# Kernel optimization log

Hardware: AMD Instinct MI355X
Metric: run time of the kernel (lower is better)

Reference implementation:

```python
import jax, jax.numpy as jnp
import numpy as np

N_SAMPLES = 10
DROPOUT_P = 0.1
EPS = 1e-12
B, F, C = 32768, 512, 1000


def setup_inputs() -> dict:
    key = jax.random.key(0)
    k1, k2, k3, k4 = jax.random.split(key, 4)
    return {
        "features": jax.random.normal(k1, (B, F), dtype=jnp.float32),
        "logits": jax.random.normal(k2, (B, C), dtype=jnp.float32),
        "W": jax.random.normal(k3, (F, C), dtype=jnp.float32) * 0.05,
        "b": jax.random.normal(k4, (C,), dtype=jnp.float32) * 0.05,
    }


def reference(features, logits, W, b):
    # `logits` is part of the provider interface but unused by this provider.
    del logits
    keep_p = 1.0 - DROPOUT_P
    mask_key = jax.random.key(42)
    # (n_samples, batch, feat) Bernoulli keep masks; inverted-dropout scaling.
    masks = jax.random.bernoulli(mask_key, keep_p, (N_SAMPLES,) + features.shape)
    dropped = jnp.where(masks, features[None] / keep_p, 0.0)  # (S, B, F)
    lgts = jnp.einsum("sbf,fc->sbc", dropped, W) + b          # (S, B, C)
    probs = jax.nn.softmax(lgts, axis=-1)                      # (S, B, C)
    mean = jnp.mean(probs, axis=0)                             # (B, C)
    # torch .var(dim=0) uses unbiased (n-1) normalization.
    var = jnp.sum((probs - mean[None]) ** 2, axis=0) / (N_SAMPLES - 1)
    total_var = jnp.sum(var, axis=-1, keepdims=True)           # (B, 1)
    # Scaler not fitted -> _normalize is identity.
    return jnp.log(total_var + EPS)
```

## Files before the change

kernel.cpp:

```cpp
#include <hip/hip_runtime.h>
#include <hip/hip_bf16.h>
#include <stdint.h>
#include <math.h>

typedef __attribute__((ext_vector_type(8))) short short8;
typedef __attribute__((ext_vector_type(4))) float f32x4;

namespace {
constexpr int kB = 32768;
constexpr int kF = 512;
constexpr int kC = 1000;
constexpr int kCpad = 1024;
constexpr int kS = 10;
constexpr int G = 8;
constexpr int M = G * kS;
constexpr int MT = M / 16;
constexpr int NTW = 8;
constexpr int WAVES = 8;
constexpr int SK = 64;
constexpr int SLICES = kF / SK;
constexpr uint32_t SLICE_BYTES = M * SK * 2;
constexpr uint32_t kKeepThr = 3865470464u;
}

__device__ __forceinline__ uint32_t rotl32(uint32_t x, uint32_t r) {
#if __has_builtin(__builtin_rotateleft32)
  return __builtin_rotateleft32(x, r);
#else
  return (x << r) | (x >> (32u - r));
#endif
}

__device__ __forceinline__ uint32_t threefry2x32_xor(uint32_t c0, uint32_t c1) {
  const uint32_t ks0 = 0u;
  const uint32_t ks1 = 42u;
  const uint32_t ks2 = 0x1BD11BDAu ^ ks0 ^ ks1;
  uint32_t x0 = c0 + ks0;
  uint32_t x1 = c1 + ks1;
#define TF_ROUND(r) { x0 += x1; x1 = rotl32(x1, r); x1 ^= x0; }
  TF_ROUND(13u) TF_ROUND(15u) TF_ROUND(26u) TF_ROUND(6u)
  x0 += ks1; x1 += ks2 + 1u;
  TF_ROUND(17u) TF_ROUND(29u) TF_ROUND(16u) TF_ROUND(24u)
  x0 += ks2; x1 += ks0 + 2u;
  TF_ROUND(13u) TF_ROUND(15u) TF_ROUND(26u) TF_ROUND(6u)
  x0 += ks0; x1 += ks1 + 3u;
  TF_ROUND(17u) TF_ROUND(29u) TF_ROUND(16u) TF_ROUND(24u)
  x0 += ks1; x1 += ks2 + 4u;
  TF_ROUND(13u) TF_ROUND(15u) TF_ROUND(26u) TF_ROUND(6u)
  x0 += ks2; x1 += ks0 + 5u;
#undef TF_ROUND
  return x0 ^ x1;
}

__device__ __forceinline__ uint32_t f2bf(float x) {
  uint32_t u = __float_as_uint(x);
  return (u + 0x7fffu + ((u >> 16) & 1u)) >> 16;
}

__device__ __forceinline__ uint32_t pack_bf16x2(float lo, float hi) {
  uint32_t r;
  asm("v_cvt_pk_bf16_f32 %0, %1, %2" : "=v"(r) : "v"(lo), "v"(hi));
  return r;
}


__global__ __launch_bounds__(256) void prep_wt(const float* __restrict__ W,
                                               ushort* __restrict__ Wt) {
  __shared__ float tile[64][65];
  const int kt = blockIdx.x * 64;
  const int ct = blockIdx.y * 64;
  const int tid = threadIdx.x;
#pragma unroll
  for (int i = 0; i < 16; ++i) {
    const int lin = i * 256 + tid;
    const int rk = lin >> 6, cc = lin & 63;
    const int gc = ct + cc;
    tile[rk][cc] = (gc < kC) ? W[(size_t)(kt + rk) * kC + gc] : 0.0f;
  }
  __syncthreads();
#pragma unroll
  for (int i = 0; i < 8; ++i) {
    const int lin = i * 256 + tid;
    const int cc = lin >> 5, kp = lin & 31;
    const int gc = ct + cc;
    const uint32_t lo = f2bf(tile[kp * 2][cc]);
    const uint32_t hi = f2bf(tile[kp * 2 + 1][cc]);
    ((uint32_t*)Wt)[(size_t)gc * (kF / 2) + (kt >> 1) + kp] = lo | (hi << 16);
  }
}

__global__ __launch_bounds__(256) void prep_bias(const float* __restrict__ b,
                                                 float* __restrict__ biasp) {
  const int i = blockIdx.x * 256 + threadIdx.x;
  if (i < kCpad) biasp[i] = (i < kC) ? b[i] : -INFINITY;
}


__global__ __launch_bounds__(512, 2) void mc_mfma_kernel(
    const float* __restrict__ features, const ushort* __restrict__ Wt,
    const float* __restrict__ biasp, float* __restrict__ out) {
  __shared__ __align__(16) ushort Abuf[2][M * SK];
  __shared__ float wred[M][9];
  __shared__ float rowinv[M];
  __shared__ float part[G][9];

  const int tid = threadIdx.x;
  const int b0 = blockIdx.x * G;
  const int wv = tid >> 6;
  const int lane = tid & 63;
  const int cp = lane & 15;
  const int gr = lane >> 4;
  const int cbase = wv * 128;

  const int fp = tid & 31;
  const int mbase = tid >> 5;
  const int gg = mbase & 7;
  const int s0 = mbase >> 3;
  char* const Ab0 = (char*)&Abuf[0][0];

  const uint32_t idx_row =
      (uint32_t)s0 * (uint32_t)(kB * kF) + (uint32_t)(b0 + gg) * kF +
      (uint32_t)(fp * 2);
  const uint32_t swz_off =
      ((uint32_t)(mbase * 128 + fp * 4)) ^ ((uint32_t)gg << 4);
  const float2* const fbase =
      (const float2*)features + ((uint32_t)(b0 + gg) * (kF / 2) + fp);

  auto gen_dword = [&](uint32_t idxb, uint32_t byteb, int i, float f0,
                       float f1) {
    const uint32_t c1 = idxb + ((uint32_t)i << 25);
    const uint32_t bits0 = threefry2x32_xor(0u, c1);
    const uint32_t bits1 = threefry2x32_xor(0u, c1 + 1u);
    const float a0 = (bits0 < kKeepThr) ? f0 : 0.0f;
    const float a1 = (bits1 < kKeepThr) ? f1 : 0.0f;
    *(uint32_t*)(Ab0 + byteb + (uint32_t)(i * 2048)) = pack_bf16x2(a0, a1);
  };

  f32x4 acc[MT][NTW];
#pragma unroll
  for (int mt = 0; mt < MT; ++mt)
#pragma unroll
    for (int nt = 0; nt < NTW; ++nt)
#pragma unroll
      for (int r = 0; r < 4; ++r) acc[mt][nt][r] = 0.0f;

  const uint32_t wbase = (uint32_t)(cbase + cp) * kF + (uint32_t)(gr * 8);
  const uint32_t aswz = (uint32_t)((cp & 7) << 4);
  const uint32_t arow = (uint32_t)(cp * 128);

  {
    const float2 fv = fbase[0];
    const float f0 = fv.x * (1.0f / 0.9f);
    const float f1 = fv.y * (1.0f / 0.9f);
#pragma unroll
    for (int i = 0; i < 5; ++i) gen_dword(idx_row, swz_off, i, f0, f1);
  }
  __syncthreads();

#pragma unroll 1
  for (int sl = 0; sl < SLICES; ++sl) {
    const uint32_t cur = (uint32_t)(sl & 1) * SLICE_BYTES;
    const uint32_t nxt = cur ^ SLICE_BYTES;
    const uint32_t wsl = wbase + (uint32_t)(sl * SK);
    const char* Ar = (const char*)Ab0 + cur;
    const bool has_next = (sl + 1 < SLICES);

    const float2 fv = fbase[((sl + 1) & 7) * 32];
    const float f0 = fv.x * (1.0f / 0.9f);
    const float f1 = fv.y * (1.0f / 0.9f);
    const uint32_t idxb = idx_row + (uint32_t)((sl + 1) * SK);
    const uint32_t byteb = nxt + swz_off;

    short8 bfA[4], bfB[4];

#pragma unroll
    for (int nt = 0; nt < 4; ++nt)
      bfA[nt] = *(const short8*)(Wt + wsl + (uint32_t)nt * 8192u);

    if (has_next) {
#pragma unroll
      for (int i = 0; i < 3; ++i) gen_dword(idxb, byteb, i, f0, f1);
    }
    __builtin_amdgcn_sched_barrier(0);

#pragma unroll
    for (int nt = 0; nt < 4; ++nt)
      bfB[nt] = *(const short8*)(Wt + wsl + (uint32_t)(nt + 4) * 8192u);

    short8 a[MT];
#pragma unroll
    for (int mt = 0; mt < MT; ++mt)
      a[mt] = *(const short8*)(Ar + (uint32_t)(mt * 2048) + arow +
                               (((uint32_t)(gr * 16)) ^ aswz));
    __builtin_amdgcn_s_setprio(1);
#pragma unroll
    for (int nt = 0; nt < 4; ++nt)
#pragma unroll
      for (int mt = 0; mt < MT; ++mt)
        acc[mt][nt] = __builtin_amdgcn_mfma_f32_16x16x32_bf16(
            a[mt], bfA[nt], acc[mt][nt], 0, 0, 0);
#pragma unroll
    for (int nt = 4; nt < 8; ++nt)
#pragma unroll
      for (int mt = 0; mt < MT; ++mt)
        acc[mt][nt] = __builtin_amdgcn_mfma_f32_16x16x32_bf16(
            a[mt], bfB[nt - 4], acc[mt][nt], 0, 0, 0);
    __builtin_amdgcn_s_setprio(0);
    __builtin_amdgcn_sched_barrier(0);

#pragma unroll
    for (int nt = 0; nt < 4; ++nt)
      bfA[nt] = *(const short8*)(Wt + wsl + 32u + (uint32_t)nt * 8192u);

    if (has_next) {
#pragma unroll
      for (int i = 3; i < 5; ++i) gen_dword(idxb, byteb, i, f0, f1);
    }
    __builtin_amdgcn_sched_barrier(0);

#pragma unroll
    for (int nt = 0; nt < 4; ++nt)
      bfB[nt] = *(const short8*)(Wt + wsl + 32u + (uint32_t)(nt + 4) * 8192u);

#pragma unroll
    for (int mt = 0; mt < MT; ++mt)
      a[mt] = *(const short8*)(Ar + (uint32_t)(mt * 2048) + arow +
                               (((uint32_t)(64 + gr * 16)) ^ aswz));
    __builtin_amdgcn_s_setprio(1);
#pragma unroll
    for (int nt = 0; nt < 4; ++nt)
#pragma unroll
      for (int mt = 0; mt < MT; ++mt)
        acc[mt][nt] = __builtin_amdgcn_mfma_f32_16x16x32_bf16(
            a[mt], bfA[nt], acc[mt][nt], 0, 0, 0);
#pragma unroll
    for (int nt = 4; nt < 8; ++nt)
#pragma unroll
      for (int mt = 0; mt < MT; ++mt)
        acc[mt][nt] = __builtin_amdgcn_mfma_f32_16x16x32_bf16(
            a[mt], bfB[nt - 4], acc[mt][nt], 0, 0, 0);
    __builtin_amdgcn_s_setprio(0);

    __syncthreads();
  }

  const float* bp = biasp + cbase + cp;
  float bias_lane[NTW];
#pragma unroll
  for (int nt = 0; nt < NTW; ++nt) bias_lane[nt] = bp[nt * 16];

  float red[MT][4];
#pragma unroll
  for (int mt = 0; mt < MT; ++mt)
#pragma unroll
    for (int r = 0; r < 4; ++r) {
      float z = 0.0f;
#pragma unroll
      for (int nt = 0; nt < NTW; ++nt) {
        const float e = __expf(acc[mt][nt][r] + bias_lane[nt]);
        acc[mt][nt][r] = e;
        z += e;
      }
      red[mt][r] = z;
    }
#pragma unroll
  for (int off = 1; off <= 8; off <<= 1)
#pragma unroll
    for (int mt = 0; mt < MT; ++mt)
#pragma unroll
      for (int r = 0; r < 4; ++r) red[mt][r] += __shfl_xor(red[mt][r], off);
  if (cp == 0) {
#pragma unroll
    for (int mt = 0; mt < MT; ++mt)
#pragma unroll
      for (int r = 0; r < 4; ++r) wred[mt * 16 + gr * 4 + r][wv] = red[mt][r];
  }
  __syncthreads();
  if (tid < M) {
    float z = 0.0f;
#pragma unroll
    for (int w = 0; w < WAVES; ++w) z += wred[tid][w];
    rowinv[tid] = 1.0f / z;
  }
  __syncthreads();

#pragma unroll
  for (int mt = 0; mt < MT; ++mt)
#pragma unroll
    for (int r = 0; r < 4; ++r) red[mt][r] = rowinv[mt * 16 + gr * 4 + r];

  float vp[4] = {0.0f, 0.0f, 0.0f, 0.0f};
#pragma unroll
  for (int nt = 0; nt < NTW; ++nt)
#pragma unroll
    for (int r = 0; r < 4; ++r) {
      float sp = 0.0f, sp2 = 0.0f;
#pragma unroll
      for (int mt = 0; mt < MT; ++mt) {
        const float p = acc[mt][nt][r] * red[mt][r];
        sp += p;
        sp2 += p * p;
      }
      sp += __shfl_xor(sp, 32);
      sp2 += __shfl_xor(sp2, 32);
      vp[r] += sp2 - sp * sp * 0.1f;
    }
#pragma unroll
  for (int off = 1; off <= 8; off <<= 1)
#pragma unroll
    for (int r = 0; r < 4; ++r) vp[r] += __shfl_xor(vp[r], off);
  if (cp == 0 && gr < 2) {
#pragma unroll
    for (int r = 0; r < 4; ++r) part[gr * 4 + r][wv] = vp[r];
  }
  __syncthreads();
  if (tid < G) {
    float t = 0.0f;
#pragma unroll
    for (int w = 0; w < WAVES; ++w) t += part[tid][w];
    t = fmaxf(t, 0.0f);
    out[b0 + tid] = logf(t * (1.0f / 9.0f) + 1e-12f);
  }
}


template <bool IS_MAX>
__device__ __forceinline__ float block_reduce(float v, float* red) {
#pragma unroll
  for (int off = 32; off >= 1; off >>= 1) {
    const float o = __shfl_xor(v, off);
    v = IS_MAX ? fmaxf(v, o) : (v + o);
  }
  const int wid = threadIdx.x >> 6;
  if ((threadIdx.x & 63) == 0) red[wid] = v;
  __syncthreads();
  float r = red[0];
#pragma unroll
  for (int w = 1; w < 4; ++w) r = IS_MAX ? fmaxf(r, red[w]) : (r + red[w]);
  __syncthreads();
  return r;
}

__global__ __launch_bounds__(256) void mc_dropout_var_kernel(
    const float* __restrict__ features, const float* __restrict__ W,
    const float* __restrict__ bias, float* __restrict__ out) {
  const int b = blockIdx.x;
  const int tid = threadIdx.x;
  __shared__ float mf[kS][kF];
  __shared__ float red[4];
  const uint32_t row_base = (uint32_t)b * (uint32_t)kF;
  for (int k = 0; k < (kS * kF) / 256; ++k) {
    const int lin = k * 256 + tid;
    const int s = lin >> 9;
    const int f = lin & (kF - 1);
    const uint32_t idx =
        (uint32_t)s * (uint32_t)(kB * kF) + row_base + (uint32_t)f;
    const uint32_t bits = threefry2x32_xor(0u, idx);
    const float u = __uint_as_float((bits >> 9) | 0x3f800000u) - 1.0f;
    const float fv = features[row_base + f];
    mf[s][f] = (u < 0.9f) ? (fv / 0.9f) : 0.0f;
  }
  __syncthreads();
  const bool active = (tid < kC / 4);
  const int c0 = tid * 4;
  float acc[kS][4];
#pragma unroll
  for (int s = 0; s < kS; ++s)
#pragma unroll
    for (int j = 0; j < 4; ++j) acc[s][j] = 0.0f;
  if (active) {
    const float* wp = W + c0;
    for (int f = 0; f < kF; f += 4) {
      float wv[4][4];
      *reinterpret_cast<float4*>(wv[0]) =
          *reinterpret_cast<const float4*>(wp + (size_t)(f + 0) * kC);
      *reinterpret_cast<float4*>(wv[1]) =
          *reinterpret_cast<const float4*>(wp + (size_t)(f + 1) * kC);
      *reinterpret_cast<float4*>(wv[2]) =
          *reinterpret_cast<const float4*>(wp + (size_t)(f + 2) * kC);
      *reinterpret_cast<float4*>(wv[3]) =
          *reinterpret_cast<const float4*>(wp + (size_t)(f + 3) * kC);
#pragma unroll
      for (int s = 0; s < kS; ++s) {
        float mm[4];
        *reinterpret_cast<float4*>(mm) =
            *reinterpret_cast<const float4*>(&mf[s][f]);
#pragma unroll
        for (int j = 0; j < 4; ++j) {
#pragma unroll
          for (int q = 0; q < 4; ++q)
            acc[s][j] = fmaf(mm[q], wv[q][j], acc[s][j]);
        }
      }
    }
  }
  float bias_r[4] = {0.f, 0.f, 0.f, 0.f};
  if (active) {
    const float4 bb = *reinterpret_cast<const float4*>(bias + c0);
    bias_r[0] = bb.x; bias_r[1] = bb.y; bias_r[2] = bb.z; bias_r[3] = bb.w;
  }
  float sum_p[4] = {0.f, 0.f, 0.f, 0.f};
  float sum_p2[4] = {0.f, 0.f, 0.f, 0.f};
#pragma unroll 1
  for (int s = 0; s < kS; ++s) {
    float l[4] = {0.f, 0.f, 0.f, 0.f};
    float lmax = -INFINITY;
    if (active) {
#pragma unroll
      for (int j = 0; j < 4; ++j) {
        l[j] = acc[s][j] + bias_r[j];
        lmax = fmaxf(lmax, l[j]);
      }
    }
    const float bmax = block_reduce<true>(lmax, red);
    float psum = 0.f;
    float p[4] = {0.f, 0.f, 0.f, 0.f};
    if (active) {
#pragma unroll
      for (int j = 0; j < 4; ++j) {
        p[j] = expf(l[j] - bmax);
        psum += p[j];
      }
    }
    const float bsum = block_reduce<false>(psum, red);
    const float inv = 1.0f / bsum;
    if (active) {
#pragma unroll
      for (int j = 0; j < 4; ++j) {
        const float pr = p[j] * inv;
        sum_p[j] += pr;
        sum_p2[j] += pr * pr;
      }
    }
  }
  float partv = 0.f;
  if (active) {
#pragma unroll
    for (int j = 0; j < 4; ++j)
      partv += (sum_p2[j] - sum_p[j] * sum_p[j] * 0.1f) * (1.0f / 9.0f);
  }
  const float total = block_reduce<false>(partv, red);
  if (tid == 0) out[b] = logf(total + 1e-12f);
}


extern "C" void kernel_launch(void* const* d_in, const int* in_sizes, int n_in,
                              void* d_out, int out_size, void* d_ws, size_t ws_size,
                              hipStream_t stream) {
  const float* features = (const float*)d_in[0];
  const float* W = (const float*)d_in[2];
  const float* bias = (const float*)d_in[3];
  float* out = (float*)d_out;

  const size_t wt_bytes = (size_t)kCpad * kF * sizeof(ushort);
  const size_t need = wt_bytes + (size_t)kCpad * sizeof(float);

  if (ws_size >= need) {
    ushort* Wt = (ushort*)d_ws;
    float* biasp = (float*)((char*)d_ws + wt_bytes);
    hipLaunchKernelGGL(prep_wt, dim3(kF / 64, kCpad / 64), dim3(256), 0, stream,
                       W, Wt);
    hipLaunchKernelGGL(prep_bias, dim3((kCpad + 255) / 256), dim3(256), 0,
                       stream, bias, biasp);
    hipLaunchKernelGGL(mc_mfma_kernel, dim3(kB / G), dim3(512), 0, stream,
                       features, Wt, biasp, out);
  } else {
    hipLaunchKernelGGL(mc_dropout_var_kernel, dim3(kB), dim3(256), 0, stream,
                       features, W, bias, out);
  }
}
```

Baseline: 672.7 us.

## Split dropout mask generation into a separate bit-packed PRNG kernel

Adds a standalone kernel that runs Threefry once per mask bit and packs the keep decisions into 32-bit words in workspace (about 21 MB). A new GEMM kernel loads each block's mask words into LDS and expands features with bit tests instead of hashing inline, and it uses larger 128-wide K slices. The aim is to take the integer-heavy PRNG work out of the MFMA main loop so it no longer competes with matrix issue. The cost is an extra launch plus a write and read of the mask buffer through global memory, and the new path only runs when the workspace is large enough.

Result: slower. 1.154 ms (+71.6%).

```diff
diff --git a/kernel.cpp b/kernel.cpp
--- a/kernel.cpp
+++ b/kernel.cpp
@@ -20,6 +20,10 @@
 constexpr int SK = 64;
 constexpr int SLICES = kF / SK;
 constexpr uint32_t SLICE_BYTES = M * SK * 2;
+constexpr int SK2 = 128;
+constexpr int SLICES2 = kF / SK2;
+constexpr uint32_t SLICE_B2 = M * SK2 * 2;
+constexpr uint32_t kMaskWords = (uint32_t)kS * kB * (kF / 32);
 constexpr uint32_t kKeepThr = 3865470464u;
 }
 
@@ -96,6 +100,220 @@
 }
 
 
+__global__ __launch_bounds__(256) void prng_masks(uint32_t* __restrict__ mw) {
+  const uint32_t t = blockIdx.x * 256u + threadIdx.x;
+#pragma unroll 1
+  for (int k = 0; k < 10; ++k) {
+    const uint32_t w = (uint32_t)k * 524288u + t;
+    const uint32_t base = w << 5;
+    uint32_t word = 0u;
+#pragma unroll
+    for (int j = 0; j < 32; ++j)
+      word |= (threefry2x32_xor(0u, base + (uint32_t)j) < kKeepThr)
+                  ? (1u << j)
+                  : 0u;
+    mw[w] = word;
+  }
+}
+
+
+__global__ __launch_bounds__(512, 2) void mc_gemm_kernel(
+    const float* __restrict__ features, const ushort* __restrict__ Wt,
+    const float* __restrict__ biasp, const uint32_t* __restrict__ maskw,
+    float* __restrict__ out) {
+  __shared__ __align__(16) ushort Abuf[2][M * SK2];
+  __shared__ uint32_t mlds[M][16];
+  __shared__ float wred[M][9];
+  __shared__ float rowinv[M];
+  __shared__ float part[G][9];
+
+  const int tid = threadIdx.x;
+  const int b0 = blockIdx.x * G;
+  const int wv = tid >> 6;
+  const int lane = tid & 63;
+  const int cp = lane & 15;
+  const int gr = lane >> 4;
+  const int cbase = wv * 128;
+  char* const Ab0 = (char*)&Abuf[0][0];
+
+  for (int w = tid; w < M * 16; w += 512) {
+    const int m = w >> 4, ww = w & 15;
+    mlds[m][ww] = maskw[((uint32_t)(m >> 3) << 19) +
+                        (uint32_t)(b0 + (m & 7)) * 16u + ww];
+  }
+
+  const int dcol = tid & 63;
+  const int rbase = tid >> 6;
+  const float2* const fptr =
+      (const float2*)features + (uint32_t)(b0 + rbase) * (kF / 2) + dcol;
+  const uint32_t wsh = (uint32_t)((dcol * 2) & 31);
+  const int mwsel = dcol >> 4;
+
+  auto exp_dword = [&](int sl, uint32_t lbase, int i, float f0, float f1) {
+    const int m = rbase + 8 * i;
+    const uint32_t mwrd = mlds[m][sl * 4 + mwsel];
+    const float a0 = (mwrd & (1u << wsh)) ? f0 : 0.0f;
+    const float a1 = (mwrd & (2u << wsh)) ? f1 : 0.0f;
+    const uint32_t byte =
+        ((uint32_t)(m * 256 + dcol * 4)) ^ ((uint32_t)(m & 15) << 4);
+    *(uint32_t*)(Ab0 + lbase + byte) = pack_bf16x2(a0, a1);
+  };
+
+  f32x4 acc[MT][NTW];
+#pragma unroll
+  for (int mt = 0; mt < MT; ++mt)
+#pragma unroll
+    for (int nt = 0; nt < NTW; ++nt)
+#pragma unroll
+      for (int r = 0; r < 4; ++r) acc[mt][nt][r] = 0.0f;
+
+  const uint32_t wbase = (uint32_t)(cbase + cp) * kF + (uint32_t)(gr * 8);
+  const uint32_t aswz = (uint32_t)(cp << 4);
+  const uint32_t arow = (uint32_t)(cp * 256);
+
+  __syncthreads();
+
+  {
+    const float2 fv = fptr[0];
+    const float f0 = fv.x * (1.0f / 0.9f);
+    const float f1 = fv.y * (1.0f / 0.9f);
+#pragma unroll
+    for (int i = 0; i < 10; ++i) exp_dword(0, 0u, i, f0, f1);
+  }
+  __syncthreads();
+
+#define KSTEP(kk, NE, IB)                                                 \
+  {                                                                       \
+    short8 bf[NTW];                                                       \
+    _Pragma("unroll")                                                     \
+    for (int nt = 0; nt < NTW; ++nt)                                      \
+      bf[nt] = *(const short8*)(Wt + wsl + (uint32_t)((kk) * 32) +        \
+                                (uint32_t)nt * 8192u);                    \
+    if (hn) {                                                             \
+      _Pragma("unroll")                                                   \
+      for (int e = 0; e < (NE); ++e)                                      \
+        exp_dword(sl + 1, nxt, (IB) + e, f0, f1);                         \
+    }                                                                     \
+    __builtin_amdgcn_sched_barrier(0);                                    \
+    short8 a[MT];                                                         \
+    _Pragma("unroll")                                                     \
+    for (int mt = 0; mt < MT; ++mt)                                       \
+      a[mt] = *(const short8*)(Ar + (uint32_t)(mt * 4096) + arow +        \
+                               (((uint32_t)((kk) * 64 + gr * 16)) ^ aswz)); \
+    __builtin_amdgcn_s_setprio(1);                                        \
+    _Pragma("unroll")                                                     \
+    for (int nt = 0; nt < NTW; ++nt)                                      \
+      _Pragma("unroll")                                                   \
+      for (int mt = 0; mt < MT; ++mt)                                     \
+        acc[mt][nt] = __builtin_amdgcn_mfma_f32_16x16x32_bf16(            \
+            a[mt], bf[nt], acc[mt][nt], 0, 0, 0);                         \
+    __builtin_amdgcn_s_setprio(0);                                        \
+  }
+
+#pragma unroll 1
+  for (int sl = 0; sl < SLICES2; ++sl) {
+    const uint32_t cur = (uint32_t)(sl & 1) * SLICE_B2;
+    const uint32_t nxt = cur ^ SLICE_B2;
+    const uint32_t wsl = wbase + (uint32_t)(sl * SK2);
+    const char* Ar = (const char*)Ab0 + cur;
+    const bool hn = (sl + 1 < SLICES2);
+
+    float f0 = 0.0f, f1 = 0.0f;
+    if (hn) {
+      const float2 fv = fptr[(sl + 1) * (SK2 / 2)];
+      f0 = fv.x * (1.0f / 0.9f);
+      f1 = fv.y * (1.0f / 0.9f);
+    }
+
+    KSTEP(0, 3, 0)
+    KSTEP(1, 3, 3)
+    KSTEP(2, 2, 6)
+    KSTEP(3, 2, 8)
+
+    __syncthreads();
+  }
+#undef KSTEP
+
+  const float* bp = biasp + cbase + cp;
+  float bias_lane[NTW];
+#pragma unroll
+  for (int nt = 0; nt < NTW; ++nt) bias_lane[nt] = bp[nt * 16];
+
+  float red[MT][4];
+#pragma unroll
+  for (int mt = 0; mt < MT; ++mt)
+#pragma unroll
+    for (int r = 0; r < 4; ++r) {
+      float z = 0.0f;
+#pragma unroll
+      for (int nt = 0; nt < NTW; ++nt) {
+        const float e = __expf(acc[mt][nt][r] + bias_lane[nt]);
+        acc[mt][nt][r] = e;
+        z += e;
+      }
+      red[mt][r] = z;
+    }
+#pragma unroll
+  for (int off = 1; off <= 8; off <<= 1)
+#pragma unroll
+    for (int mt = 0; mt < MT; ++mt)
+#pragma unroll
+      for (int r = 0; r < 4; ++r) red[mt][r] += __shfl_xor(red[mt][r], off);
+  if (cp == 0) {
+#pragma unroll
+    for (int mt = 0; mt < MT; ++mt)
+#pragma unroll
+      for (int r = 0; r < 4; ++r) wred[mt * 16 + gr * 4 + r][wv] = red[mt][r];
+  }
+  __syncthreads();
+  if (tid < M) {
+    float z = 0.0f;
+#pragma unroll
+    for (int w = 0; w < WAVES; ++w) z += wred[tid][w];
+    rowinv[tid] = 1.0f / z;
+  }
+  __syncthreads();
+
+#pragma unroll
+  for (int mt = 0; mt < MT; ++mt)
+#pragma unroll
+    for (int r = 0; r < 4; ++r) red[mt][r] = rowinv[mt * 16 + gr * 4 + r];
+
+  float vp[4] = {0.0f, 0.0f, 0.0f, 0.0f};
+#pragma unroll
+  for (int nt = 0; nt < NTW; ++nt)
+#pragma unroll
+    for (int r = 0; r < 4; ++r) {
+      float sp = 0.0f, sp2 = 0.0f;
+#pragma unroll
+      for (int mt = 0; mt < MT; ++mt) {
+        const float p = acc[mt][nt][r] * red[mt][r];
+        sp += p;
+        sp2 += p * p;
+      }
+      sp += __shfl_xor(sp, 32);
+      sp2 += __shfl_xor(sp2, 32);
+      vp[r] += sp2 - sp * sp * 0.1f;
+    }
+#pragma unroll
+  for (int off = 1; off <= 8; off <<= 1)
+#pragma unroll
+    for (int r = 0; r < 4; ++r) vp[r] += __shfl_xor(vp[r], off);
+  if (cp == 0 && gr < 2) {
+#pragma unroll
+    for (int r = 0; r < 4; ++r) part[gr * 4 + r][wv] = vp[r];
+  }
+  __syncthreads();
+  if (tid < G) {
+    float t = 0.0f;
+#pragma unroll
+    for (int w = 0; w < WAVES; ++w) t += part[tid][w];
+    t = fmaxf(t, 0.0f);
+    out[b0 + tid] = logf(t * (1.0f / 9.0f) + 1e-12f);
+  }
+}
+
+
 __global__ __launch_bounds__(512, 2) void mc_mfma_kernel(
     const float* __restrict__ features, const ushort* __restrict__ Wt,
     const float* __restrict__ biasp, float* __restrict__ out) {
@@ -176,17 +394,15 @@
 #pragma unroll
     for (int nt = 0; nt < 4; ++nt)
       bfA[nt] = *(const short8*)(Wt + wsl + (uint32_t)nt * 8192u);
-
     if (has_next) {
-#pragma unroll
-      for (int i = 0; i < 3; ++i) gen_dword(idxb, byteb, i, f0, f1);
+      gen_dword(idxb, byteb, 0, f0, f1);
+      gen_dword(idxb, byteb, 1, f0, f1);
+      gen_dword(idxb, byteb, 2, f0, f1);
     }
     __builtin_amdgcn_sched_barrier(0);
-
 #pragma unroll
     for (int nt = 0; nt < 4; ++nt)
       bfB[nt] = *(const short8*)(Wt + wsl + (uint32_t)(nt + 4) * 8192u);
-
     short8 a[MT];
 #pragma unroll
     for (int mt = 0; mt < MT; ++mt)
@@ -211,17 +427,14 @@
 #pragma unroll
     for (int nt = 0; nt < 4; ++nt)
       bfA[nt] = *(const short8*)(Wt + wsl + 32u + (uint32_t)nt * 8192u);
-
     if (has_next) {
-#pragma unroll
-      for (int i = 3; i < 5; ++i) gen_dword(idxb, byteb, i, f0, f1);
+      gen_dword(idxb, byteb, 3, f0, f1);
+      gen_dword(idxb, byteb, 4, f0, f1);
     }
     __builtin_amdgcn_sched_barrier(0);
-
 #pragma unroll
     for (int nt = 0; nt < 4; ++nt)
       bfB[nt] = *(const short8*)(Wt + wsl + 32u + (uint32_t)(nt + 4) * 8192u);
-
 #pragma unroll
     for (int mt = 0; mt < MT; ++mt)
       a[mt] = *(const short8*)(Ar + (uint32_t)(mt * 2048) + arow +
@@ -453,17 +666,27 @@
   float* out = (float*)d_out;
 
   const size_t wt_bytes = (size_t)kCpad * kF * sizeof(ushort);
-  const size_t need = wt_bytes + (size_t)kCpad * sizeof(float);
-
-  if (ws_size >= need) {
+  const size_t bias_bytes = (size_t)kCpad * sizeof(float);
+  const size_t mask_bytes = (size_t)kMaskWords * sizeof(uint32_t);
+  const size_t need_fused = wt_bytes + bias_bytes;
+  const size_t need_split = need_fused + mask_bytes;
+
+  if (ws_size >= need_fused) {
     ushort* Wt = (ushort*)d_ws;
     float* biasp = (float*)((char*)d_ws + wt_bytes);
     hipLaunchKernelGGL(prep_wt, dim3(kF / 64, kCpad / 64), dim3(256), 0, stream,
                        W, Wt);
     hipLaunchKernelGGL(prep_bias, dim3((kCpad + 255) / 256), dim3(256), 0,
                        stream, bias, biasp);
-    hipLaunchKernelGGL(mc_mfma_kernel, dim3(kB / G), dim3(512), 0, stream,
-                       features, Wt, biasp, out);
+    if (ws_size >= need_split) {
+      uint32_t* maskw = (uint32_t*)((char*)d_ws + wt_bytes + bias_bytes);
+      hipLaunchKernelGGL(prng_masks, dim3(2048), dim3(256), 0, stream, maskw);
+      hipLaunchKernelGGL(mc_gemm_kernel, dim3(kB / G), dim3(512), 0, stream,
+                         features, Wt, biasp, maskw, out);
+    } else {
+      hipLaunchKernelGGL(mc_mfma_kernel, dim3(kB / G), dim3(512), 0, stream,
+                         features, Wt, biasp, out);
+    }
   } else {
     hipLaunchKernelGGL(mc_dropout_var_kernel, dim3(kB), dim3(256), 0, stream,
                        features, W, bias, out);
```
